# Kernel optimization log

Measured on AMD Instinct MI355X. Metric: run time of the kernel, lower is better.

The kernel has to match this reference:

```python
import jax, jax.numpy as jnp
import numpy as np

SIGMA_AGG = 0.5
SIGMA_DIS = 3.0
ALPHA = 0.5
BETA = 0.25
EPS = 1e-5
K_MAX = 8  # number of kernel/text instances per image; labels in {0..K_MAX}, 0 = background


def setup_inputs() -> dict:
    key = jax.random.key(0)
    ks = jax.random.split(key, 7)
    B, C, H, W = 16, 4, 640, 640
    return dict(
        pred_regions=jax.random.normal(ks[0], (B, 1, H, W), jnp.float32),
        regions_gt=jax.random.randint(ks[1], (B, 1, H, W), 0, 2).astype(jnp.float32),
        pred_kernels=jax.random.normal(ks[2], (B, 1, H, W), jnp.float32),
        kernels_gt=jax.random.randint(ks[3], (B, 1, H, W), 0, 2).astype(jnp.float32),
        pred_similarities=jax.random.normal(ks[4], (B, C, H, W), jnp.float32),
        text_mask_ndi_labels=jax.random.randint(ks[5], (B, H, W), 0, K_MAX + 1, dtype=jnp.int32),
        kernel_mask_ndi_labels=jax.random.randint(ks[6], (B, H, W), 0, K_MAX + 1, dtype=jnp.int32),
    )


def _dice_loss(pred, gt, eps):
    # sigmoid -> per-sample dice, summed over batch (matches Text/KernelDiceLoss)
    p = jax.nn.sigmoid(pred).reshape(pred.shape[0], -1)
    g = gt.reshape(gt.shape[0], -1)
    inter = jnp.sum(p * g, axis=1)
    denom = (jnp.sum(p * p, axis=1) + eps) + (jnp.sum(g * g, axis=1) + eps)
    dice = (2.0 * inter + eps) / denom
    return jnp.sum(1.0 - dice)


def _agg_dis_single(sim, tlab, klab):
    # sim: (C, H, W); tlab/klab: (H, W) int instance labels (0 = background)
    C = sim.shape[0]
    sim = sim.reshape(C, -1)
    tlab = tlab.reshape(-1)
    klab = klab.reshape(-1)
    nseg = K_MAX + 1

    s2 = jnp.sum(sim * sim, axis=0)  # per-pixel squared feature norm, (N,)
    ones = jnp.ones_like(s2)
    ck = jax.ops.segment_sum(ones, klab, num_segments=nseg)  # kernel cardinalities
    ct = jax.ops.segment_sum(ones, tlab, num_segments=nseg)  # text cardinalities

    # Aggregation: || sim*1[T==i] - sim*1[K==i]/(ck_i+1) ||_F per instance i.
    # Per pixel, nonzero only for i = tlab[p] or i = klab[p]:
    inv = 1.0 / (ck + 1.0)
    same = tlab == klab
    coef_t = jnp.where(same, (1.0 - inv[klab]) ** 2, 1.0)  # contributes to instance tlab
    coef_k = jnp.where(same, 0.0, inv[klab] ** 2)          # contributes to instance klab
    n2 = (jax.ops.segment_sum(s2 * coef_t, tlab, num_segments=nseg)
          + jax.ops.segment_sum(s2 * coef_k, klab, num_segments=nseg))
    norm = jnp.sqrt(n2[1:])  # drop background segment 0
    # NOTE: torch.max(scalar, 0)[0] on a 0-d tensor is identity (no clamp) - reproduced here.
    l_agg = jnp.sum(jnp.log((norm - SIGMA_AGG) ** 2 + 1.0) / (ct[1:] + 1.0))

    # Discrimination: kernel masks are disjoint, so
    # ||mu_i - mu_j||_F^2 = a_i + a_j with a_i = sum_{K==i} s2 / (ck_i + 0.001)^2
    a = jax.ops.segment_sum(s2, klab, num_segments=nseg)[1:] / (ck[1:] + 0.001) ** 2
    pair = SIGMA_DIS - jnp.sqrt(a[:, None] + a[None, :])
    val = jnp.log(pair ** 2 + 1.0)
    triu = jnp.triu(jnp.ones((K_MAX, K_MAX), bool), 1)
    l_dis = jnp.sum(jnp.where(triu, val, 0.0)) / (K_MAX * (K_MAX - 1))
    return l_agg, l_dis


def reference(pred_regions, regions_gt, pred_kernels, kernels_gt,
              pred_similarities, text_mask_ndi_labels, kernel_mask_ndi_labels):
    # OHEM mask is computed in the torch code but never used by TextDiceLoss, so it is omitted.
    loss_regions = _dice_loss(pred_regions, regions_gt, EPS)
    loss_kernel = _dice_loss(pred_kernels, kernels_gt, EPS)
    l_agg, l_dis = jax.vmap(_agg_dis_single)(pred_similarities,
                                             text_mask_ndi_labels,
                                             kernel_mask_ndi_labels)
    loss_aggregation = jnp.sum(l_agg)
    loss_discrimination = jnp.sum(l_dis)
    loss = loss_regions + ALPHA * loss_kernel + BETA * (loss_aggregation + loss_discrimination)
    return (loss, loss_regions, loss_kernel, loss_aggregation, loss_discrimination)
```

## Files before the change

kernel.cpp:

```cpp
#include <hip/hip_runtime.h>
#include <math.h>


#define NSEG 9
#define NACC 51
#define NBATCH 16
#define EPSF 1e-5f
#define G 5
#define BPB 80

typedef float  vfloat4 __attribute__((ext_vector_type(4)));
typedef int    vint4   __attribute__((ext_vector_type(4)));

__device__ __forceinline__ float wave_reduce_sum(float v) {
#pragma unroll
    for (int off = 32; off > 0; off >>= 1)
        v += __shfl_down(v, off, 64);
    return v;
}

__device__ __forceinline__ float sigm(float x) {
    return 1.0f / (1.0f + __expf(-x));
}

__device__ __forceinline__ vfloat4 nt_load4(const float* p) {
    return __builtin_nontemporal_load((const vfloat4*)p);
}
__device__ __forceinline__ vint4 nt_load4i(const int* p) {
    return __builtin_nontemporal_load((const vint4*)p);
}

__global__ __launch_bounds__(256, 5) void pan_main(
    const float* __restrict__ pred_r, const float* __restrict__ gt_r,
    const float* __restrict__ pred_k, const float* __restrict__ gt_k,
    const float* __restrict__ sim,
    const int* __restrict__ tlab, const int* __restrict__ klab,
    float* __restrict__ ws, int npix)
{
    const int tid = threadIdx.x;
    const int b = blockIdx.y;
    const int base = b * npix;
    const int sbase = b * 4 * npix;
    const int i0 = blockIdx.x * (256 * G) + tid;

    float St_[8], Sk_[8], Ss_[8];
    unsigned ct_[8], ck_[8];
#pragma unroll
    for (int s = 0; s < 8; ++s) {
        St_[s] = 0.0f; Sk_[s] = 0.0f; Ss_[s] = 0.0f;
        ct_[s] = 0u; ck_[s] = 0u;
    }
    float rpg = 0.0f, rpp = 0.0f, rgg = 0.0f;
    float kpg = 0.0f, kpp = 0.0f, kgg = 0.0f;

#pragma unroll 1
    for (int g = 0; g < G; ++g) {
        const int e = (i0 + g * 256) * 4;

        const vfloat4 pr = nt_load4(pred_r + base + e);
        const vfloat4 gr = nt_load4(gt_r + base + e);
        const vfloat4 pk = nt_load4(pred_k + base + e);
        const vfloat4 gk = nt_load4(gt_k + base + e);
        const vfloat4 c0 = nt_load4(sim + sbase + e);
        const vfloat4 c1 = nt_load4(sim + sbase + npix + e);
        const vfloat4 c2 = nt_load4(sim + sbase + 2 * npix + e);
        const vfloat4 c3 = nt_load4(sim + sbase + 3 * npix + e);
        const vint4 tl = nt_load4i(tlab + base + e);
        const vint4 kl = nt_load4i(klab + base + e);

        {
            float p;
            p = sigm(pr.x); rpg += p * gr.x; rpp += p * p; rgg += gr.x;
            p = sigm(pr.y); rpg += p * gr.y; rpp += p * p; rgg += gr.y;
            p = sigm(pr.z); rpg += p * gr.z; rpp += p * p; rgg += gr.z;
            p = sigm(pr.w); rpg += p * gr.w; rpp += p * p; rgg += gr.w;
            p = sigm(pk.x); kpg += p * gk.x; kpp += p * p; kgg += gk.x;
            p = sigm(pk.y); kpg += p * gk.y; kpp += p * p; kgg += gk.y;
            p = sigm(pk.z); kpg += p * gk.z; kpp += p * p; kgg += gk.z;
            p = sigm(pk.w); kpg += p * gk.w; kpp += p * p; kgg += gk.w;
        }

        const float s2x = c0.x * c0.x + c1.x * c1.x + c2.x * c2.x + c3.x * c3.x;
        const float s2y = c0.y * c0.y + c1.y * c1.y + c2.y * c2.y + c3.y * c3.y;
        const float s2z = c0.z * c0.z + c1.z * c1.z + c2.z * c2.z + c3.z * c3.z;
        const float s2w = c0.w * c0.w + c1.w * c1.w + c2.w * c2.w + c3.w * c3.w;

#define DO_COMP(TL, KL, S2)                                      \
        {                                                        \
            bool tt = ((TL) == s);                               \
            bool kk = ((KL) == s);                               \
            ct_[s - 1] += (unsigned)__popcll(__ballot(tt));      \
            ck_[s - 1] += (unsigned)__popcll(__ballot(kk));      \
            St_[s - 1] += tt ? (S2) : 0.0f;                      \
            Sk_[s - 1] += kk ? (S2) : 0.0f;                      \
            Ss_[s - 1] += (tt && kk) ? (S2) : 0.0f;              \
        }

#pragma unroll
        for (int s = 1; s <= 8; ++s) {
            DO_COMP(tl.x, kl.x, s2x);
            DO_COMP(tl.y, kl.y, s2y);
            DO_COMP(tl.z, kl.z, s2z);
            DO_COMP(tl.w, kl.w, s2w);
        }
#undef DO_COMP
    }

    __shared__ float red[4][NACC];
    const int lane = tid & 63;
    const int wv = tid >> 6;

#pragma unroll
    for (int s = 0; s < 8; ++s) {
        float v;
        v = wave_reduce_sum(St_[s]); if (lane == 0) red[wv][19 + s] = v;
        v = wave_reduce_sum(Sk_[s]); if (lane == 0) red[wv][28 + s] = v;
        v = wave_reduce_sum(Ss_[s]); if (lane == 0) red[wv][37 + s] = v;
    }
    {
        float v;
        v = wave_reduce_sum(rpg); if (lane == 0) red[wv][45] = v;
        v = wave_reduce_sum(rpp); if (lane == 0) red[wv][46] = v;
        v = wave_reduce_sum(rgg); if (lane == 0) red[wv][47] = v;
        v = wave_reduce_sum(kpg); if (lane == 0) red[wv][48] = v;
        v = wave_reduce_sum(kpp); if (lane == 0) red[wv][49] = v;
        v = wave_reduce_sum(kgg); if (lane == 0) red[wv][50] = v;
    }
    if (lane == 0) {
#pragma unroll
        for (int s = 0; s < 8; ++s) {
            red[wv][1 + s] = (float)ct_[s];
            red[wv][10 + s] = (float)ck_[s];
        }
        red[wv][0] = 0.0f; red[wv][9] = 0.0f; red[wv][18] = 0.0f;
        red[wv][27] = 0.0f; red[wv][36] = 0.0f;
    }
    __syncthreads();
    if (tid < NACC) {
        float s = red[0][tid] + red[1][tid] + red[2][tid] + red[3][tid];
        atomicAdd(&ws[b * NACC + tid], s);
    }
}

__global__ __launch_bounds__(64) void pan_finalize(
    const float* __restrict__ ws, float* __restrict__ out)
{
    const int b = threadIdx.x;
    float dice_r = 0.0f, dice_k = 0.0f, lagg = 0.0f, ldis = 0.0f;

    if (b < NBATCH) {
        const float* w = ws + b * NACC;
        {
            float pg = w[45], pp = w[46], gg = w[47];
            dice_r = 1.0f - (2.0f * pg + EPSF) / ((pp + EPSF) + (gg + EPSF));
            pg = w[48]; pp = w[49]; gg = w[50];
            dice_k = 1.0f - (2.0f * pg + EPSF) / ((pp + EPSF) + (gg + EPSF));
        }
        float a[8];
#pragma unroll
        for (int i = 1; i < NSEG; ++i) {
            float ct = w[i], ck = w[NSEG + i];
            float St = w[2 * NSEG + i], Sk = w[3 * NSEG + i], Ss = w[4 * NSEG + i];
            float inv = 1.0f / (ck + 1.0f);
            float omi = 1.0f - inv;
            float n2 = omi * omi * Ss + (St - Ss) + inv * inv * (Sk - Ss);
            float nrm = sqrtf(n2);
            float d = nrm - 0.5f;
            lagg += logf(d * d + 1.0f) / (ct + 1.0f);
            float ckd = ck + 0.001f;
            a[i - 1] = Sk / (ckd * ckd);
        }
#pragma unroll
        for (int i = 0; i < 8; ++i) {
#pragma unroll
            for (int j = i + 1; j < 8; ++j) {
                float pair = 3.0f - sqrtf(a[i] + a[j]);
                ldis += logf(pair * pair + 1.0f);
            }
        }
        ldis *= (1.0f / 56.0f);
    }

    dice_r = wave_reduce_sum(dice_r);
    dice_k = wave_reduce_sum(dice_k);
    lagg = wave_reduce_sum(lagg);
    ldis = wave_reduce_sum(ldis);

    if (threadIdx.x == 0) {
        float loss = dice_r + 0.5f * dice_k + 0.25f * (lagg + ldis);
        out[0] = loss;
        out[1] = dice_r;
        out[2] = dice_k;
        out[3] = lagg;
        out[4] = ldis;
    }
}

extern "C" void kernel_launch(void* const* d_in, const int* in_sizes, int n_in,
                              void* d_out, int out_size, void* d_ws, size_t ws_size,
                              hipStream_t stream) {
    const float* pred_r = (const float*)d_in[0];
    const float* gt_r   = (const float*)d_in[1];
    const float* pred_k = (const float*)d_in[2];
    const float* gt_k   = (const float*)d_in[3];
    const float* sim    = (const float*)d_in[4];
    const int*   tlab   = (const int*)d_in[5];
    const int*   klab   = (const int*)d_in[6];
    float* out = (float*)d_out;
    float* ws  = (float*)d_ws;

    const int npix = in_sizes[0] / NBATCH;

    (void)hipMemsetAsync(ws, 0, NBATCH * NACC * sizeof(float), stream);

    dim3 grid(BPB, NBATCH);
    pan_main<<<grid, 256, 0, stream>>>(pred_r, gt_r, pred_k, gt_k, sim,
                                       tlab, klab, ws, npix);
    pan_finalize<<<1, 64, 0, stream>>>(ws, out);
}
```

Measured before the change: 254.2 us.

## Split dice and instance-statistics work into separate block sets with staggered tiles

The grid doubles so one half of the blocks handles the similarity/label segment statistics and the other half handles the two dice reductions. Tile indices are rotated per batch and offset between the two halves, so concurrently running blocks touch different address ranges. The aim is to shorten per-block work and lower register pressure in the heavy segment path, giving more parallelism for a memory-bound stream. The cost is extra block launches and duplicated reduction and atomic overhead.

```diff
diff --git a/kernel.cpp b/kernel.cpp
--- a/kernel.cpp
+++ b/kernel.cpp
@@ -40,105 +40,127 @@
     const int tid = threadIdx.x;
     const int b = blockIdx.y;
     const int base = b * npix;
-    const int sbase = b * 4 * npix;
-    const int i0 = blockIdx.x * (256 * G) + tid;
-
-    float St_[8], Sk_[8], Ss_[8];
-    unsigned ct_[8], ck_[8];
-#pragma unroll
-    for (int s = 0; s < 8; ++s) {
-        St_[s] = 0.0f; Sk_[s] = 0.0f; Ss_[s] = 0.0f;
-        ct_[s] = 0u; ck_[s] = 0u;
-    }
-    float rpg = 0.0f, rpp = 0.0f, rgg = 0.0f;
-    float kpg = 0.0f, kpp = 0.0f, kgg = 0.0f;
-
-#pragma unroll 1
-    for (int g = 0; g < G; ++g) {
-        const int e = (i0 + g * 256) * 4;
-
-        const vfloat4 pr = nt_load4(pred_r + base + e);
-        const vfloat4 gr = nt_load4(gt_r + base + e);
-        const vfloat4 pk = nt_load4(pred_k + base + e);
-        const vfloat4 gk = nt_load4(gt_k + base + e);
-        const vfloat4 c0 = nt_load4(sim + sbase + e);
-        const vfloat4 c1 = nt_load4(sim + sbase + npix + e);
-        const vfloat4 c2 = nt_load4(sim + sbase + 2 * npix + e);
-        const vfloat4 c3 = nt_load4(sim + sbase + 3 * npix + e);
-        const vint4 tl = nt_load4i(tlab + base + e);
-        const vint4 kl = nt_load4i(klab + base + e);
-
-        {
-            float p;
-            p = sigm(pr.x); rpg += p * gr.x; rpp += p * p; rgg += gr.x;
-            p = sigm(pr.y); rpg += p * gr.y; rpp += p * p; rgg += gr.y;
-            p = sigm(pr.z); rpg += p * gr.z; rpp += p * p; rgg += gr.z;
-            p = sigm(pr.w); rpg += p * gr.w; rpp += p * p; rgg += gr.w;
-            p = sigm(pk.x); kpg += p * gk.x; kpp += p * p; kgg += gk.x;
-            p = sigm(pk.y); kpg += p * gk.y; kpp += p * p; kgg += gk.y;
-            p = sigm(pk.z); kpg += p * gk.z; kpp += p * p; kgg += gk.z;
-            p = sigm(pk.w); kpg += p * gk.w; kpp += p * p; kgg += gk.w;
-        }
-
-        const float s2x = c0.x * c0.x + c1.x * c1.x + c2.x * c2.x + c3.x * c3.x;
-        const float s2y = c0.y * c0.y + c1.y * c1.y + c2.y * c2.y + c3.y * c3.y;
-        const float s2z = c0.z * c0.z + c1.z * c1.z + c2.z * c2.z + c3.z * c3.z;
-        const float s2w = c0.w * c0.w + c1.w * c1.w + c2.w * c2.w + c3.w * c3.w;
-
-#define DO_COMP(TL, KL, S2)                                      \
-        {                                                        \
-            bool tt = ((TL) == s);                               \
-            bool kk = ((KL) == s);                               \
-            ct_[s - 1] += (unsigned)__popcll(__ballot(tt));      \
-            ck_[s - 1] += (unsigned)__popcll(__ballot(kk));      \
-            St_[s - 1] += tt ? (S2) : 0.0f;                      \
-            Sk_[s - 1] += kk ? (S2) : 0.0f;                      \
-            Ss_[s - 1] += (tt && kk) ? (S2) : 0.0f;              \
-        }
-
-#pragma unroll
-        for (int s = 1; s <= 8; ++s) {
-            DO_COMP(tl.x, kl.x, s2x);
-            DO_COMP(tl.y, kl.y, s2y);
-            DO_COMP(tl.z, kl.z, s2z);
-            DO_COMP(tl.w, kl.w, s2w);
-        }
-#undef DO_COMP
-    }
-
-    __shared__ float red[4][NACC];
     const int lane = tid & 63;
     const int wv = tid >> 6;
 
-#pragma unroll
-    for (int s = 0; s < 8; ++s) {
-        float v;
-        v = wave_reduce_sum(St_[s]); if (lane == 0) red[wv][19 + s] = v;
-        v = wave_reduce_sum(Sk_[s]); if (lane == 0) red[wv][28 + s] = v;
-        v = wave_reduce_sum(Ss_[s]); if (lane == 0) red[wv][37 + s] = v;
-    }
-    {
-        float v;
-        v = wave_reduce_sum(rpg); if (lane == 0) red[wv][45] = v;
-        v = wave_reduce_sum(rpp); if (lane == 0) red[wv][46] = v;
-        v = wave_reduce_sum(rgg); if (lane == 0) red[wv][47] = v;
-        v = wave_reduce_sum(kpg); if (lane == 0) red[wv][48] = v;
-        v = wave_reduce_sum(kpp); if (lane == 0) red[wv][49] = v;
-        v = wave_reduce_sum(kgg); if (lane == 0) red[wv][50] = v;
-    }
-    if (lane == 0) {
+    __shared__ float red[4][NACC];
+
+    if (blockIdx.x < BPB) {
+        const int sbase = b * 4 * npix;
+        int bx = blockIdx.x + 5 * b;
+        if (bx >= BPB) bx -= BPB;
+        const int i0 = bx * (256 * G) + tid;
+
+        float St_[8], Sk_[8], Ss_[8];
+        unsigned ct_[8], ck_[8];
 #pragma unroll
         for (int s = 0; s < 8; ++s) {
-            red[wv][1 + s] = (float)ct_[s];
-            red[wv][10 + s] = (float)ck_[s];
-        }
-        red[wv][0] = 0.0f; red[wv][9] = 0.0f; red[wv][18] = 0.0f;
-        red[wv][27] = 0.0f; red[wv][36] = 0.0f;
-    }
-    __syncthreads();
-    if (tid < NACC) {
-        float s = red[0][tid] + red[1][tid] + red[2][tid] + red[3][tid];
-        atomicAdd(&ws[b * NACC + tid], s);
+            St_[s] = 0.0f; Sk_[s] = 0.0f; Ss_[s] = 0.0f;
+            ct_[s] = 0u; ck_[s] = 0u;
+        }
+
+#pragma unroll 1
+        for (int g = 0; g < G; ++g) {
+            const int e = (i0 + g * 256) * 4;
+            const vfloat4 c0 = nt_load4(sim + sbase + e);
+            const vfloat4 c1 = nt_load4(sim + sbase + npix + e);
+            const vfloat4 c2 = nt_load4(sim + sbase + 2 * npix + e);
+            const vfloat4 c3 = nt_load4(sim + sbase + 3 * npix + e);
+            const vint4 tl = nt_load4i(tlab + base + e);
+            const vint4 kl = nt_load4i(klab + base + e);
+
+            const float s2x = c0.x*c0.x + c1.x*c1.x + c2.x*c2.x + c3.x*c3.x;
+            const float s2y = c0.y*c0.y + c1.y*c1.y + c2.y*c2.y + c3.y*c3.y;
+            const float s2z = c0.z*c0.z + c1.z*c1.z + c2.z*c2.z + c3.z*c3.z;
+            const float s2w = c0.w*c0.w + c1.w*c1.w + c2.w*c2.w + c3.w*c3.w;
+
+#define DO_COMP(TL, KL, S2)                                      \
+            {                                                    \
+                bool tt = ((TL) == s);                           \
+                bool kk = ((KL) == s);                           \
+                ct_[s - 1] += (unsigned)__popcll(__ballot(tt));  \
+                ck_[s - 1] += (unsigned)__popcll(__ballot(kk));  \
+                St_[s - 1] += tt ? (S2) : 0.0f;                  \
+                Sk_[s - 1] += kk ? (S2) : 0.0f;                  \
+                Ss_[s - 1] += (tt && kk) ? (S2) : 0.0f;          \
+            }
+#pragma unroll
+            for (int s = 1; s <= 8; ++s) {
+                DO_COMP(tl.x, kl.x, s2x);
+                DO_COMP(tl.y, kl.y, s2y);
+                DO_COMP(tl.z, kl.z, s2z);
+                DO_COMP(tl.w, kl.w, s2w);
+            }
+#undef DO_COMP
+        }
+
+#pragma unroll
+        for (int s = 0; s < 8; ++s) {
+            float v;
+            v = wave_reduce_sum(St_[s]); if (lane == 0) red[wv][19 + s] = v;
+            v = wave_reduce_sum(Sk_[s]); if (lane == 0) red[wv][28 + s] = v;
+            v = wave_reduce_sum(Ss_[s]); if (lane == 0) red[wv][37 + s] = v;
+        }
+        if (lane == 0) {
+#pragma unroll
+            for (int s = 0; s < 8; ++s) {
+                red[wv][1 + s] = (float)ct_[s];
+                red[wv][10 + s] = (float)ck_[s];
+            }
+            red[wv][0] = 0.0f; red[wv][9] = 0.0f; red[wv][18] = 0.0f;
+            red[wv][27] = 0.0f; red[wv][36] = 0.0f;
+        }
+        __syncthreads();
+        if (tid < 45) {
+            float s = red[0][tid] + red[1][tid] + red[2][tid] + red[3][tid];
+            atomicAdd(&ws[b * NACC + tid], s);
+        }
+    } else {
+        int bx = (blockIdx.x - BPB) + 5 * b + 40;
+        bx %= BPB;
+        const int i0 = bx * (256 * G) + tid;
+
+        float rpg = 0.0f, rpp = 0.0f, rgg = 0.0f;
+        float kpg = 0.0f, kpp = 0.0f, kgg = 0.0f;
+
+#pragma unroll 1
+        for (int g = 0; g < G; ++g) {
+            const int e = (i0 + g * 256) * 4;
+            const vfloat4 pr = nt_load4(pred_r + base + e);
+            const vfloat4 gr = nt_load4(gt_r + base + e);
+            {
+                float p;
+                p = sigm(pr.x); rpg += p * gr.x; rpp += p * p; rgg += gr.x;
+                p = sigm(pr.y); rpg += p * gr.y; rpp += p * p; rgg += gr.y;
+                p = sigm(pr.z); rpg += p * gr.z; rpp += p * p; rgg += gr.z;
+                p = sigm(pr.w); rpg += p * gr.w; rpp += p * p; rgg += gr.w;
+            }
+            const vfloat4 pk = nt_load4(pred_k + base + e);
+            const vfloat4 gk = nt_load4(gt_k + base + e);
+            {
+                float p;
+                p = sigm(pk.x); kpg += p * gk.x; kpp += p * p; kgg += gk.x;
+                p = sigm(pk.y); kpg += p * gk.y; kpp += p * p; kgg += gk.y;
+                p = sigm(pk.z); kpg += p * gk.z; kpp += p * p; kgg += gk.z;
+                p = sigm(pk.w); kpg += p * gk.w; kpp += p * p; kgg += gk.w;
+            }
+        }
+
+        {
+            float v;
+            v = wave_reduce_sum(rpg); if (lane == 0) red[wv][45] = v;
+            v = wave_reduce_sum(rpp); if (lane == 0) red[wv][46] = v;
+            v = wave_reduce_sum(rgg); if (lane == 0) red[wv][47] = v;
+            v = wave_reduce_sum(kpg); if (lane == 0) red[wv][48] = v;
+            v = wave_reduce_sum(kpp); if (lane == 0) red[wv][49] = v;
+            v = wave_reduce_sum(kgg); if (lane == 0) red[wv][50] = v;
+        }
+        __syncthreads();
+        if (tid < 6) {
+            int q = 45 + tid;
+            float s = red[0][q] + red[1][q] + red[2][q] + red[3][q];
+            atomicAdd(&ws[b * NACC + q], s);
+        }
     }
 }
 
@@ -213,7 +235,7 @@
 
     (void)hipMemsetAsync(ws, 0, NBATCH * NACC * sizeof(float), stream);
 
-    dim3 grid(BPB, NBATCH);
+    dim3 grid(2 * BPB, NBATCH);
     pan_main<<<grid, 256, 0, stream>>>(pred_r, gt_r, pred_k, gt_k, sim,
                                        tlab, klab, ws, npix);
     pan_finalize<<<1, 64, 0, stream>>>(ws, out);
```

New measurement: 253.1 us. Within noise of the previous version (-0.5%).
